# Kernel tuning notes

Measured on AMD Instinct MI355X. Metric: run time of the kernel, lower is better.

The kernel has to match this reference:

```python
import jax, jax.numpy as jnp
import numpy as np

MAX_SEQ, D, VOCAB, N_LAYERS = 2048, 256, 240, 6
DH = 64.0  # scale used inside RelativeGlobalAttention
BATCH = 4


def _pos_embedding():
    # sin(pow(pos*1e-5, i/D) - pi/2 * ((i+1)%2)), exactly as in __init__
    pos = np.arange(MAX_SEQ, dtype=np.float64)[:, None]
    i = np.arange(D, dtype=np.float64)[None, :]
    ang = np.power(pos * 1e-5, i / D) - np.pi * 0.5 * ((i + 1) % 2)
    return jnp.asarray(np.sin(ang), dtype=jnp.float32)  # [L, D]


def _skew(QE):
    # pad a zero column in front, reshape [B,L,L+1]->[B,L+1,L], drop first row
    B, L, _ = QE.shape
    cat = jnp.concatenate([jnp.zeros((B, L, 1), QE.dtype), QE], axis=2)
    return cat.reshape(B, L + 1, L)[:, 1:, :]


def _rel_attn(x, Wq, Wk, Wv):
    Q = x @ Wq  # [B,L,D]
    K = x @ Wk
    V = x @ Wv
    QE = jnp.einsum('bld,bmd->blm', Q, K - Q)      # Q @ (K-Q)^T
    Srel = _skew(QE)
    QKt = jnp.einsum('bld,bmd->blm', Q, K)
    scores = (QKt + Srel) / jnp.sqrt(jnp.asarray(DH, x.dtype))
    probs = jax.nn.softmax(scores, axis=-1)        # no causal mask in source
    return probs @ V


def setup_inputs() -> dict:
    key = jax.random.key(0)
    ks = jax.random.split(key, 16)
    s = 1.0 / np.sqrt(D)
    mk = lambda k, shape, sc: (jax.random.normal(k, shape, jnp.float32) * sc)
    inp = {
        'tokens': jax.random.randint(ks[0], (BATCH, MAX_SEQ), 0, VOCAB),
        'embed_table': mk(ks[1], (VOCAB, D), 0.05),
        'Wq1': mk(ks[2], (N_LAYERS, D, D), s),
        'Wk1': mk(ks[3], (N_LAYERS, D, D), s),
        'Wv1': mk(ks[4], (N_LAYERS, D, D), s),
        'Wq2': mk(ks[5], (N_LAYERS, D, D), s),
        'Wk2': mk(ks[6], (N_LAYERS, D, D), s),
        'Wv2': mk(ks[7], (N_LAYERS, D, D), s),
        'Wf1': mk(ks[8], (N_LAYERS, D, D), s),
        'bf1': jnp.zeros((N_LAYERS, D), jnp.float32),
        'Wf2': mk(ks[9], (N_LAYERS, D, D), s),
        'bf2': jnp.zeros((N_LAYERS, D), jnp.float32),
        'Wfc': mk(ks[10], (MAX_SEQ * D, VOCAB), 1.0 / np.sqrt(MAX_SEQ * D)),
        'bfc': jnp.zeros((VOCAB,), jnp.float32),
    }
    return inp


def reference(tokens, embed_table, Wq1, Wk1, Wv1, Wq2, Wk2, Wv2,
              Wf1, bf1, Wf2, bf2, Wfc, bfc):
    x = embed_table[tokens] + _pos_embedding()[None]  # [B,L,D]
    for i in range(N_LAYERS):
        x = _rel_attn(x, Wq1[i], Wk1[i], Wv1[i]) + x
        x = _rel_attn(x, Wq2[i], Wk2[i], Wv2[i]) + x
        h = jax.nn.leaky_relu(x @ Wf1[i] + bf1[i], negative_slope=0.2)
        x = h @ Wf2[i] + bf2[i]
        # NOTE: BatchNorm layers exist in source but are never called in _decoder
    flat = x.reshape(x.shape[0], -1)  # [B, L*D]
    return jax.nn.softmax(flat @ Wfc + bfc, axis=-1)  # [B, vocab]
```

## Files before the change

kernel.cpp:

```cpp
#include <hip/hip_runtime.h>
#include <hip/hip_fp16.h>

typedef unsigned short u16;
typedef unsigned int   u32;

#define BB 4
#define LL 2048
#define DD 256
#define VV 240
#define NLAYERS 6

static constexpr long BLD = (long)BB * LL * DD;
static constexpr long LD_ = (long)LL * DD;
static constexpr long LxL = (long)LL * LL;
static constexpr long BLL = (long)BB * LxL;

typedef _Float16 h8  __attribute__((ext_vector_type(8)));
typedef _Float16 h2v __attribute__((ext_vector_type(2)));
typedef float  f32x4 __attribute__((ext_vector_type(4)));

__device__ __forceinline__ u16 f2h(float f) {
    _Float16 h = (_Float16)f;
    return __builtin_bit_cast(u16, h);
}
__device__ __forceinline__ float h2f(u16 u) {
    return (float)__builtin_bit_cast(_Float16, u);
}

__device__ __forceinline__ void gl16(const void* g, void* l) {
    __builtin_amdgcn_global_load_lds((const __attribute__((address_space(1))) void*)g,
                                     (__attribute__((address_space(3))) void*)l, 16, 0, 0);
}

__global__ __launch_bounds__(256)
void embed_kernel(const int* __restrict__ tokens, const float* __restrict__ table,
                  float* __restrict__ x, u16* __restrict__ xh)
{
    long idx = (long)blockIdx.x * 256 + threadIdx.x;
    if (idx >= BLD) return;
    int i  = (int)(idx & (DD - 1));
    long bl = idx >> 8;
    int l  = (int)(bl & (LL - 1));
    int tok = tokens[bl];
    float base = (float)l * 1e-5f;
    float p = powf(base, (float)i * (1.0f / (float)DD));
    float ang = p - ((i & 1) ? 0.0f : 1.57079632679489662f);
    float v = table[(long)tok * DD + i] + sinf(ang);
    x[idx] = v;
    xh[idx] = f2h(v);
}

__global__ __launch_bounds__(256)
void wconv(const float* __restrict__ W, u16* __restrict__ Wt, long lstride)
{
    int blk = blockIdx.x;
    int m  = blk >> 6;
    int ti = (blk >> 3) & 7;
    int tj = blk & 7;
    const float* src = W + (long)m * 65536;
    u16* dst = Wt + (long)m * lstride;
    __shared__ float tile[32][33];
    int t = threadIdx.x;
    int c = t & 31, r8 = t >> 5;
    #pragma unroll
    for (int p = 0; p < 4; ++p) {
        int r = r8 + p * 8;
        tile[r][c] = src[(long)(ti * 32 + r) * 256 + tj * 32 + c];
    }
    __syncthreads();
    #pragma unroll
    for (int p = 0; p < 4; ++p) {
        int n = r8 + p * 8;
        dst[(long)(tj * 32 + n) * 256 + ti * 32 + c] = f2h(tile[c][n]);
    }
}

__global__ __launch_bounds__(256)
void sub_f16(u16* __restrict__ kk, const u16* __restrict__ q)
{
    long i = (long)blockIdx.x * 256 + threadIdx.x;
    uint4 kv = ((const uint4*)kk)[i];
    uint4 qv = ((const uint4*)q)[i];
    u32* kp = (u32*)&kv; const u32* qp = (const u32*)&qv;
    #pragma unroll
    for (int j = 0; j < 4; ++j) {
        h2v a = __builtin_bit_cast(h2v, kp[j]);
        h2v b = __builtin_bit_cast(h2v, qp[j]);
        h2v e = a - b;
        kp[j] = __builtin_bit_cast(u32, e);
    }
    ((uint4*)kk)[i] = kv;
}

template<int EPI, int BM, int BN>
__global__ __launch_bounds__(256)
void gemm_mfma(const u16* __restrict__ A, const u16* __restrict__ B,
               const float* __restrict__ bias, const float* __restrict__ Cres,
               float* __restrict__ Cf, u16* __restrict__ Ch,
               u16* __restrict__ Ch2, u16* __restrict__ Ch3,
               int M, int N, int K, int ldA,
               long sA, long sB, long sC)
{
    constexpr int FM = BM / 32, FN = BN / 32;
    __shared__ u16 As[BM * 32];
    __shared__ u16 Bs[BN * 32];
    const int bz = blockIdx.z;
    A += (long)bz * sA;
    B += (long)bz * sB;
    if constexpr (EPI & 4)  Cres += (long)bz * sC;
    if constexpr (EPI & 8)  Cf   += (long)bz * sC;
    if constexpr ((EPI & 16) && !(EPI & (32 | 64))) Ch += (long)bz * sC;
    const int bm = blockIdx.y * BM;
    const int bn = blockIdx.x * BN;
    const int t = threadIdx.x;
    const int lane = t & 63, wave = t >> 6;
    const int wm = (wave >> 1) * (BM / 2), wn = (wave & 1) * (BN / 2);

    f32x4 acc[FM][FN];
    #pragma unroll
    for (int i = 0; i < FM; ++i)
        #pragma unroll
        for (int j = 0; j < FN; ++j)
            acc[i][j] = (f32x4){0.f, 0.f, 0.f, 0.f};

    const u16* gA0 = A + (long)(bm + (t >> 2)) * ldA + (t & 3) * 8;
    const u16* gB0 = B + (long)(bn + (t >> 2)) * K + (t & 3) * 8;
    u16* lA0 = As + wave * 512;
    u16* lB0 = Bs + wave * 512;

    const int arow = wm + (lane & 15);
    const int brow = wn + (lane & 15);
    const int ko = (lane >> 4) * 8;

    for (int k0 = 0; k0 < K; k0 += 32) {
        __syncthreads();
        gl16(gA0, lA0);
        if constexpr (BM == 128) gl16(gA0 + 64L * ldA, As + 2048 + wave * 512);
        gl16(gB0, lB0);
        if constexpr (BN == 128) gl16(gB0 + 64L * K, Bs + 2048 + wave * 512);
        gA0 += 32; gB0 += 32;
        __syncthreads();
        h8 af[FM], bf[FN];
        #pragma unroll
        for (int i = 0; i < FM; ++i) af[i] = *(const h8*)&As[(arow + i * 16) * 32 + ko];
        #pragma unroll
        for (int j = 0; j < FN; ++j) bf[j] = *(const h8*)&Bs[(brow + j * 16) * 32 + ko];
        #pragma unroll
        for (int i = 0; i < FM; ++i)
            #pragma unroll
            for (int j = 0; j < FN; ++j)
                acc[i][j] = __builtin_amdgcn_mfma_f32_16x16x32_f16(af[i], bf[j], acc[i][j], 0, 0, 0);
    }

    const int colc = lane & 15;
    const int rowb = (lane >> 4) * 4;
    if constexpr (EPI & 64) {
        const int seg = bn >> 8;
        const int nb  = bn & 255;
        if (seg < 2) {
            u16* dst = seg ? Ch2 : Ch;
            #pragma unroll
            for (int i = 0; i < FM; ++i)
                #pragma unroll
                for (int j = 0; j < FN; ++j) {
                    int nn = nb + wn + j * 16 + colc;
                    #pragma unroll
                    for (int r = 0; r < 4; ++r) {
                        long row = bm + wm + i * 16 + rowb + r;
                        dst[row * DD + nn] = f2h(acc[i][j][r]);
                    }
                }
        } else {
            #pragma unroll
            for (int i = 0; i < FM; ++i) {
                int r0 = bm + wm + i * 16 + rowb;
                int b  = r0 >> 11;
                int m0 = r0 & (LL - 1);
                #pragma unroll
                for (int j = 0; j < FN; ++j) {
                    int nn = nb + wn + j * 16 + colc;
                    f32x4 v = acc[i][j];
                    ushort4 pk;
                    pk.x = f2h(v.x); pk.y = f2h(v.y); pk.z = f2h(v.z); pk.w = f2h(v.w);
                    *(ushort4*)&Ch3[((long)b * DD + nn) * LL + m0] = pk;
                }
            }
        }
    } else if constexpr (EPI & 32) {
        #pragma unroll
        for (int i = 0; i < FM; ++i) {
            int r0 = bm + wm + i * 16 + rowb;
            int b  = r0 >> 11;
            int m0 = r0 & (LL - 1);
            #pragma unroll
            for (int j = 0; j < FN; ++j) {
                int n = bn + wn + j * 16 + colc;
                f32x4 v = acc[i][j];
                ushort4 pk;
                pk.x = f2h(v.x); pk.y = f2h(v.y); pk.z = f2h(v.z); pk.w = f2h(v.w);
                *(ushort4*)&Ch[((long)b * DD + n) * LL + m0] = pk;
            }
        }
    } else {
        #pragma unroll
        for (int i = 0; i < FM; ++i) {
            #pragma unroll
            for (int j = 0; j < FN; ++j) {
                int n = bn + wn + j * 16 + colc;
                float bv = (EPI & 1) ? bias[n] : 0.f;
                #pragma unroll
                for (int r = 0; r < 4; ++r) {
                    long row = bm + wm + i * 16 + rowb + r;
                    float val = acc[i][j][r] + bv;
                    if (EPI & 2) val = (val >= 0.f) ? val : 0.2f * val;
                    long off = row * (long)N + n;
                    if (EPI & 4) val += Cres[off];
                    if (EPI & 8) Cf[off] = val;
                    if (EPI & 16) Ch[off] = f2h(val);
                }
            }
        }
    }
}

__global__ __launch_bounds__(256)
void skew_softmax(u16* __restrict__ S1, const u16* __restrict__ QE)
{
    const int bi = blockIdx.x;
    const int b = bi >> 11;
    const int i = bi & (LL - 1);
    u16* srow = S1 + (long)bi * LL;
    const u16* qe_i  = QE + ((long)b * LL + i) * LL;
    const u16* qe_i1 = qe_i + ((i + 1 < LL) ? LL : 0);
    const int t = threadIdx.x;

    uint4 sv = ((const uint4*)srow)[t];
    const u16* se = (const u16*)&sv;
    float vals[8];
    float mx = -1e30f;
    #pragma unroll
    for (int j = 0; j < 8; ++j) {
        int m = t * 8 + j;
        float srel;
        if (m <= i)            srel = h2f(qe_i[m - i + (LL - 1)]);
        else if (m == i + 1)   srel = 0.f;
        else                   srel = h2f(qe_i1[m - i - 2]);
        float s = (h2f(se[j]) + srel) * 0.125f;
        vals[j] = s;
        mx = fmaxf(mx, s);
    }
    #pragma unroll
    for (int off = 32; off >= 1; off >>= 1)
        mx = fmaxf(mx, __shfl_xor(mx, off, 64));
    __shared__ float redm[4], reds[4];
    const int wid = t >> 6;
    if ((t & 63) == 0) redm[wid] = mx;
    __syncthreads();
    mx = fmaxf(fmaxf(redm[0], redm[1]), fmaxf(redm[2], redm[3]));

    float sum = 0.f;
    #pragma unroll
    for (int j = 0; j < 8; ++j) { vals[j] = expf(vals[j] - mx); sum += vals[j]; }
    #pragma unroll
    for (int off = 32; off >= 1; off >>= 1)
        sum += __shfl_xor(sum, off, 64);
    if ((t & 63) == 0) reds[wid] = sum;
    __syncthreads();
    sum = reds[0] + reds[1] + reds[2] + reds[3];
    float inv = 1.0f / sum;
    uint4 ov;
    u16* oe = (u16*)&ov;
    #pragma unroll
    for (int j = 0; j < 8; ++j) oe[j] = f2h(vals[j] * inv);
    ((uint4*)srow)[t] = ov;
}

__global__ __launch_bounds__(960)
void fc_partial(const float* __restrict__ x, const float* __restrict__ W,
                float* __restrict__ part)
{
    const int v = threadIdx.x;
    const int b = threadIdx.y;
    const int chunk = blockIdx.x;
    const int KC = (int)(LD_ / 256);
    const long k0 = (long)chunk * KC;
    const float* xb = x + (long)b * LD_ + k0;
    const float* Wp = W + k0 * VV + v;
    float acc = 0.f;
    #pragma unroll 4
    for (int k2 = 0; k2 < KC; ++k2)
        acc = fmaf(xb[k2], Wp[(long)k2 * VV], acc);
    part[((long)chunk * BB + b) * VV + v] = acc;
}

__global__ __launch_bounds__(960)
void fc_finish(const float* __restrict__ part, const float* __restrict__ bias,
               float* __restrict__ out)
{
    const int v = threadIdx.x, b = threadIdx.y;
    float acc = bias[v];
    for (int c = 0; c < 256; ++c)
        acc += part[((long)c * BB + b) * VV + v];
    __shared__ float lds[BB][VV];
    __shared__ float mxs[BB], sms[BB];
    lds[b][v] = acc;
    __syncthreads();
    if (v == 0) {
        float m = -1e30f;
        for (int j = 0; j < VV; ++j) m = fmaxf(m, lds[b][j]);
        float s = 0.f;
        for (int j = 0; j < VV; ++j) s += expf(lds[b][j] - m);
        mxs[b] = m; sms[b] = s;
    }
    __syncthreads();
    out[b * VV + v] = expf(lds[b][v] - mxs[b]) / sms[b];
}

extern "C" void kernel_launch(void* const* d_in, const int* in_sizes, int n_in,
                              void* d_out, int out_size, void* d_ws, size_t ws_size,
                              hipStream_t stream)
{
    const int*   tokens = (const int*)d_in[0];
    const float* table  = (const float*)d_in[1];
    const float* Wq1 = (const float*)d_in[2];
    const float* Wk1 = (const float*)d_in[3];
    const float* Wv1 = (const float*)d_in[4];
    const float* Wq2 = (const float*)d_in[5];
    const float* Wk2 = (const float*)d_in[6];
    const float* Wv2 = (const float*)d_in[7];
    const float* Wf1 = (const float*)d_in[8];
    const float* bf1 = (const float*)d_in[9];
    const float* Wf2 = (const float*)d_in[10];
    const float* bf2 = (const float*)d_in[11];
    const float* Wfc = (const float*)d_in[12];
    const float* bfc = (const float*)d_in[13];

    char* p = (char*)d_ws;
    float* x  = (float*)p; p += BLD * 4;
    u16* xh = (u16*)p;     p += BLD * 2;
    u16* qb = (u16*)p;     p += BLD * 2;
    u16* kb = (u16*)p;     p += BLD * 2;
    u16* vt = (u16*)p;     p += BLD * 2;
    u16* S1 = (u16*)p;     p += BLL * 2;
    u16* QE = (u16*)p;     p += BLL * 2;
    u16* qkvw = (u16*)p;   p += 12L * 3 * 65536 * 2;
    u16* fw = (u16*)p;     p += 12L * 65536 * 2;
    float* part = (float*)p;
    u16* hb = qb;

    wconv<<<384, 256, 0, stream>>>(Wq1, qkvw + 0L * 65536,            3 * 65536);
    wconv<<<384, 256, 0, stream>>>(Wk1, qkvw + 1L * 65536,            3 * 65536);
    wconv<<<384, 256, 0, stream>>>(Wv1, qkvw + 2L * 65536,            3 * 65536);
    wconv<<<384, 256, 0, stream>>>(Wq2, qkvw + 18L * 65536,           3 * 65536);
    wconv<<<384, 256, 0, stream>>>(Wk2, qkvw + 18L * 65536 + 65536,   3 * 65536);
    wconv<<<384, 256, 0, stream>>>(Wv2, qkvw + 18L * 65536 + 2 * 65536, 3 * 65536);
    wconv<<<384, 256, 0, stream>>>(Wf1, fw, 65536);
    wconv<<<384, 256, 0, stream>>>(Wf2, fw + 6L * 65536, 65536);

    embed_kernel<<<(int)((BLD + 255) / 256), 256, 0, stream>>>(tokens, table, x, xh);

    const dim3 gqkv(6, 64, 1);
    const dim3 gscore(16, 16, BB);
    const dim3 gpv(4, 32, BB);
    const dim3 gffn(4, 128, 1);

    for (int layer = 0; layer < NLAYERS; ++layer) {
        for (int half = 0; half < 2; ++half) {
            const u16* wqkv = qkvw + ((long)(half * 6 + layer)) * 3 * 65536;
            gemm_mfma<64, 128, 128><<<gqkv, 256, 0, stream>>>(
                xh, wqkv, nullptr, nullptr, nullptr, qb, kb, vt,
                BB * LL, 768, DD, DD, 0, 0, 0);
            gemm_mfma<16, 128, 128><<<gscore, 256, 0, stream>>>(
                qb, kb, nullptr, nullptr, nullptr, S1, nullptr, nullptr,
                LL, LL, DD, DD, LD_, LD_, LxL);
            sub_f16<<<(int)(BLD / 8 / 256), 256, 0, stream>>>(kb, qb);
            gemm_mfma<16, 128, 128><<<gscore, 256, 0, stream>>>(
                qb, kb, nullptr, nullptr, nullptr, QE, nullptr, nullptr,
                LL, LL, DD, DD, LD_, LD_, LxL);
            skew_softmax<<<BB * LL, 256, 0, stream>>>(S1, QE);
            gemm_mfma<4 | 8 | 16, 64, 64><<<gpv, 256, 0, stream>>>(
                S1, vt, nullptr, x, x, xh, nullptr, nullptr,
                LL, DD, LL, LL, LxL, LD_, LD_);
        }
        gemm_mfma<1 | 2 | 16, 64, 64><<<gffn, 256, 0, stream>>>(
            xh, fw + (long)layer * 65536, bf1 + layer * DD, nullptr,
            nullptr, hb, nullptr, nullptr, BB * LL, DD, DD, DD, 0, 0, 0);
        gemm_mfma<1 | 8 | 16, 64, 64><<<gffn, 256, 0, stream>>>(
            hb, fw + (long)(6 + layer) * 65536, bf2 + layer * DD, nullptr,
            x, xh, nullptr, nullptr, BB * LL, DD, DD, DD, 0, 0, 0);
    }

    fc_partial<<<256, dim3(VV, BB, 1), 0, stream>>>(x, Wfc, part);
    fc_finish<<<1, dim3(VV, BB, 1), 0, stream>>>(part, bfc, (float*)d_out);
}
```

Measured before the change: 1.912 ms.

## Fold K-Q into weights, fuse both score GEMMs, double-buffer GEMM LDS

Computes K-Q directly as x@(Wk-Wq) by adding a difference weight to the fused projection GEMM, which removes the separate fp16 subtraction kernel. The two score GEMMs (Q@K^T and Q@(K-Q)^T) become one launch with twice the grid, each block picking its B operand and output by column range. The GEMM main loop now double-buffers its LDS tiles so the next K-slice load is issued before the current MFMAs, with one barrier per iteration instead of two. This trades a little extra projection work and rounding differences in E for fewer launches and some load/compute overlap.

```diff
diff --git a/kernel.cpp b/kernel.cpp
--- a/kernel.cpp
+++ b/kernel.cpp
@@ -16,7 +16,6 @@
 static constexpr long BLL = (long)BB * LxL;
 
 typedef _Float16 h8  __attribute__((ext_vector_type(8)));
-typedef _Float16 h2v __attribute__((ext_vector_type(2)));
 typedef float  f32x4 __attribute__((ext_vector_type(4)));
 
 __device__ __forceinline__ u16 f2h(float f) {
@@ -50,8 +49,10 @@
     xh[idx] = f2h(v);
 }
 
+template<bool DIFF>
 __global__ __launch_bounds__(256)
-void wconv(const float* __restrict__ W, u16* __restrict__ Wt, long lstride)
+void wconv(const float* __restrict__ W, const float* __restrict__ Wsub,
+           u16* __restrict__ Wt, long lstride)
 {
     int blk = blockIdx.x;
     int m  = blk >> 6;
@@ -65,7 +66,10 @@
     #pragma unroll
     for (int p = 0; p < 4; ++p) {
         int r = r8 + p * 8;
-        tile[r][c] = src[(long)(ti * 32 + r) * 256 + tj * 32 + c];
+        long off = (long)(ti * 32 + r) * 256 + tj * 32 + c;
+        float v = src[off];
+        if constexpr (DIFF) v -= Wsub[(long)m * 65536 + off];
+        tile[r][c] = v;
     }
     __syncthreads();
     #pragma unroll
@@ -75,43 +79,36 @@
     }
 }
 
-__global__ __launch_bounds__(256)
-void sub_f16(u16* __restrict__ kk, const u16* __restrict__ q)
-{
-    long i = (long)blockIdx.x * 256 + threadIdx.x;
-    uint4 kv = ((const uint4*)kk)[i];
-    uint4 qv = ((const uint4*)q)[i];
-    u32* kp = (u32*)&kv; const u32* qp = (const u32*)&qv;
-    #pragma unroll
-    for (int j = 0; j < 4; ++j) {
-        h2v a = __builtin_bit_cast(h2v, kp[j]);
-        h2v b = __builtin_bit_cast(h2v, qp[j]);
-        h2v e = a - b;
-        kp[j] = __builtin_bit_cast(u32, e);
-    }
-    ((uint4*)kk)[i] = kv;
-}
-
 template<int EPI, int BM, int BN>
 __global__ __launch_bounds__(256)
 void gemm_mfma(const u16* __restrict__ A, const u16* __restrict__ B,
+               const u16* __restrict__ B2,
                const float* __restrict__ bias, const float* __restrict__ Cres,
                float* __restrict__ Cf, u16* __restrict__ Ch,
-               u16* __restrict__ Ch2, u16* __restrict__ Ch3,
+               u16* __restrict__ Ch2, u16* __restrict__ Ch3, u16* __restrict__ Ch4,
                int M, int N, int K, int ldA,
                long sA, long sB, long sC)
 {
     constexpr int FM = BM / 32, FN = BN / 32;
-    __shared__ u16 As[BM * 32];
-    __shared__ u16 Bs[BN * 32];
+    __shared__ u16 As[2][BM * 32];
+    __shared__ u16 Bs[2][BN * 32];
     const int bz = blockIdx.z;
     A += (long)bz * sA;
-    B += (long)bz * sB;
+    const int bm = blockIdx.y * BM;
+    const int bn = blockIdx.x * BN;
+    int bnb = bn;
+    const u16* Bp;
+    if constexpr (EPI & 128) {
+        Bp = (bn >= LL) ? B2 : B;
+        if (bn >= LL) bnb = bn - LL;
+        Bp += (long)bz * sB;
+    } else {
+        Bp = B + (long)bz * sB;
+    }
     if constexpr (EPI & 4)  Cres += (long)bz * sC;
     if constexpr (EPI & 8)  Cf   += (long)bz * sC;
-    if constexpr ((EPI & 16) && !(EPI & (32 | 64))) Ch += (long)bz * sC;
-    const int bm = blockIdx.y * BM;
-    const int bn = blockIdx.x * BN;
+    if constexpr ((EPI & 16) && !(EPI & (64 | 128))) Ch += (long)bz * sC;
+
     const int t = threadIdx.x;
     const int lane = t & 63, wave = t >> 6;
     const int wm = (wave >> 1) * (BM / 2), wn = (wave & 1) * (BN / 2);
@@ -123,42 +120,51 @@
         for (int j = 0; j < FN; ++j)
             acc[i][j] = (f32x4){0.f, 0.f, 0.f, 0.f};
 
-    const u16* gA0 = A + (long)(bm + (t >> 2)) * ldA + (t & 3) * 8;
-    const u16* gB0 = B + (long)(bn + (t >> 2)) * K + (t & 3) * 8;
-    u16* lA0 = As + wave * 512;
-    u16* lB0 = Bs + wave * 512;
+    const u16* gA0 = A  + (long)(bm  + (t >> 2)) * ldA + (t & 3) * 8;
+    const u16* gB0 = Bp + (long)(bnb + (t >> 2)) * K   + (t & 3) * 8;
 
     const int arow = wm + (lane & 15);
     const int brow = wn + (lane & 15);
     const int ko = (lane >> 4) * 8;
 
+    #define STAGE(buf, koff) do {                                              \
+        gl16(gA0 + (koff), &As[buf][wave * 512]);                              \
+        if constexpr (BM == 128) gl16(gA0 + 64L * ldA + (koff),                \
+                                      &As[buf][2048 + wave * 512]);            \
+        gl16(gB0 + (koff), &Bs[buf][wave * 512]);                              \
+        if constexpr (BN == 128) gl16(gB0 + 64L * K + (koff),                  \
+                                      &Bs[buf][2048 + wave * 512]);            \
+    } while (0)
+
+    STAGE(0, 0);
+    int cur = 0;
     for (int k0 = 0; k0 < K; k0 += 32) {
         __syncthreads();
-        gl16(gA0, lA0);
-        if constexpr (BM == 128) gl16(gA0 + 64L * ldA, As + 2048 + wave * 512);
-        gl16(gB0, lB0);
-        if constexpr (BN == 128) gl16(gB0 + 64L * K, Bs + 2048 + wave * 512);
-        gA0 += 32; gB0 += 32;
-        __syncthreads();
+        if (k0 + 32 < K) {
+            if (cur) STAGE(0, k0 + 32);
+            else     STAGE(1, k0 + 32);
+        }
         h8 af[FM], bf[FN];
         #pragma unroll
-        for (int i = 0; i < FM; ++i) af[i] = *(const h8*)&As[(arow + i * 16) * 32 + ko];
-        #pragma unroll
-        for (int j = 0; j < FN; ++j) bf[j] = *(const h8*)&Bs[(brow + j * 16) * 32 + ko];
+        for (int i = 0; i < FM; ++i) af[i] = *(const h8*)&As[cur][(arow + i * 16) * 32 + ko];
+        #pragma unroll
+        for (int j = 0; j < FN; ++j) bf[j] = *(const h8*)&Bs[cur][(brow + j * 16) * 32 + ko];
         #pragma unroll
         for (int i = 0; i < FM; ++i)
             #pragma unroll
             for (int j = 0; j < FN; ++j)
                 acc[i][j] = __builtin_amdgcn_mfma_f32_16x16x32_f16(af[i], bf[j], acc[i][j], 0, 0, 0);
-    }
+        cur ^= 1;
+    }
+    #undef STAGE
 
     const int colc = lane & 15;
     const int rowb = (lane >> 4) * 4;
     if constexpr (EPI & 64) {
         const int seg = bn >> 8;
         const int nb  = bn & 255;
-        if (seg < 2) {
-            u16* dst = seg ? Ch2 : Ch;
+        if (seg < 3) {
+            u16* dst = (seg == 0) ? Ch : ((seg == 1) ? Ch2 : Ch3);
             #pragma unroll
             for (int i = 0; i < FM; ++i)
                 #pragma unroll
@@ -182,25 +188,24 @@
                     f32x4 v = acc[i][j];
                     ushort4 pk;
                     pk.x = f2h(v.x); pk.y = f2h(v.y); pk.z = f2h(v.z); pk.w = f2h(v.w);
-                    *(ushort4*)&Ch3[((long)b * DD + nn) * LL + m0] = pk;
+                    *(ushort4*)&Ch4[((long)b * DD + nn) * LL + m0] = pk;
                 }
             }
         }
-    } else if constexpr (EPI & 32) {
-        #pragma unroll
-        for (int i = 0; i < FM; ++i) {
-            int r0 = bm + wm + i * 16 + rowb;
-            int b  = r0 >> 11;
-            int m0 = r0 & (LL - 1);
+    } else if constexpr (EPI & 128) {
+        u16* dst = ((bn >= LL) ? Ch2 : Ch) + (long)bz * sC;
+        const int nb = bn & (LL - 1);
+        #pragma unroll
+        for (int i = 0; i < FM; ++i)
             #pragma unroll
             for (int j = 0; j < FN; ++j) {
-                int n = bn + wn + j * 16 + colc;
-                f32x4 v = acc[i][j];
-                ushort4 pk;
-                pk.x = f2h(v.x); pk.y = f2h(v.y); pk.z = f2h(v.z); pk.w = f2h(v.w);
-                *(ushort4*)&Ch[((long)b * DD + n) * LL + m0] = pk;
+                int n = nb + wn + j * 16 + colc;
+                #pragma unroll
+                for (int r = 0; r < 4; ++r) {
+                    long row = bm + wm + i * 16 + rowb + r;
+                    dst[row * LL + n] = f2h(acc[i][j][r]);
+                }
             }
-        }
     } else {
         #pragma unroll
         for (int i = 0; i < FM; ++i) {
@@ -340,54 +345,54 @@
     u16* xh = (u16*)p;     p += BLD * 2;
     u16* qb = (u16*)p;     p += BLD * 2;
     u16* kb = (u16*)p;     p += BLD * 2;
+    u16* eb = (u16*)p;     p += BLD * 2;
     u16* vt = (u16*)p;     p += BLD * 2;
     u16* S1 = (u16*)p;     p += BLL * 2;
     u16* QE = (u16*)p;     p += BLL * 2;
-    u16* qkvw = (u16*)p;   p += 12L * 3 * 65536 * 2;
+    u16* qkevw = (u16*)p;  p += 12L * 4 * 65536 * 2;
     u16* fw = (u16*)p;     p += 12L * 65536 * 2;
     float* part = (float*)p;
     u16* hb = qb;
 
-    wconv<<<384, 256, 0, stream>>>(Wq1, qkvw + 0L * 65536,            3 * 65536);
-    wconv<<<384, 256, 0, stream>>>(Wk1, qkvw + 1L * 65536,            3 * 65536);
-    wconv<<<384, 256, 0, stream>>>(Wv1, qkvw + 2L * 65536,            3 * 65536);
-    wconv<<<384, 256, 0, stream>>>(Wq2, qkvw + 18L * 65536,           3 * 65536);
-    wconv<<<384, 256, 0, stream>>>(Wk2, qkvw + 18L * 65536 + 65536,   3 * 65536);
-    wconv<<<384, 256, 0, stream>>>(Wv2, qkvw + 18L * 65536 + 2 * 65536, 3 * 65536);
-    wconv<<<384, 256, 0, stream>>>(Wf1, fw, 65536);
-    wconv<<<384, 256, 0, stream>>>(Wf2, fw + 6L * 65536, 65536);
+    const long LS = 4 * 65536;
+    wconv<false><<<384, 256, 0, stream>>>(Wq1, nullptr, qkevw + 0L * 65536, LS);
+    wconv<false><<<384, 256, 0, stream>>>(Wk1, nullptr, qkevw + 1L * 65536, LS);
+    wconv<true ><<<384, 256, 0, stream>>>(Wk1, Wq1,     qkevw + 2L * 65536, LS);
+    wconv<false><<<384, 256, 0, stream>>>(Wv1, nullptr, qkevw + 3L * 65536, LS);
+    wconv<false><<<384, 256, 0, stream>>>(Wq2, nullptr, qkevw + 24L * 65536, LS);
+    wconv<true ><<<384, 256, 0, stream>>>(Wk2, Wq2,     qkevw + 24L * 65536 + 2 * 65536, LS);
+    wconv<false><<<384, 256, 0, stream>>>(Wk2, nullptr, qkevw + 24L * 65536 + 1 * 65536, LS);
+    wconv<false><<<384, 256, 0, stream>>>(Wv2, nullptr, qkevw + 24L * 65536 + 3 * 65536, LS);
+    wconv<false><<<384, 256, 0, stream>>>(Wf1, nullptr, fw, 65536);
+    wconv<false><<<384, 256, 0, stream>>>(Wf2, nullptr, fw + 6L * 65536, 65536);
 
     embed_kernel<<<(int)((BLD + 255) / 256), 256, 0, stream>>>(tokens, table, x, xh);
 
-    const dim3 gqkv(6, 64, 1);
-    const dim3 gscore(16, 16, BB);
+    const dim3 gqkev(8, 64, 1);
+    const dim3 gscore(32, 16, BB);
     const dim3 gpv(4, 32, BB);
     const dim3 gffn(4, 128, 1);
 
     for (int layer = 0; layer < NLAYERS; ++layer) {
         for (int half = 0; half < 2; ++half) {
-            const u16* wqkv = qkvw + ((long)(half * 6 + layer)) * 3 * 65536;
-            gemm_mfma<64, 128, 128><<<gqkv, 256, 0, stream>>>(
-                xh, wqkv, nullptr, nullptr, nullptr, qb, kb, vt,
-                BB * LL, 768, DD, DD, 0, 0, 0);
-            gemm_mfma<16, 128, 128><<<gscore, 256, 0, stream>>>(
-                qb, kb, nullptr, nullptr, nullptr, S1, nullptr, nullptr,
-                LL, LL, DD, DD, LD_, LD_, LxL);
-            sub_f16<<<(int)(BLD / 8 / 256), 256, 0, stream>>>(kb, qb);
-            gemm_mfma<16, 128, 128><<<gscore, 256, 0, stream>>>(
-                qb, kb, nullptr, nullptr, nullptr, QE, nullptr, nullptr,
+            const u16* wqkev = qkevw + ((long)(half * 6 + layer)) * LS;
+            gemm_mfma<64, 128, 128><<<gqkev, 256, 0, stream>>>(
+                xh, wqkev, nullptr, nullptr, nullptr, nullptr, qb, kb, eb, vt,
+                BB * LL, 1024, DD, DD, 0, 0, 0);
+            gemm_mfma<128, 128, 128><<<gscore, 256, 0, stream>>>(
+                qb, kb, eb, nullptr, nullptr, nullptr, S1, QE, nullptr, nullptr,
                 LL, LL, DD, DD, LD_, LD_, LxL);
             skew_softmax<<<BB * LL, 256, 0, stream>>>(S1, QE);
             gemm_mfma<4 | 8 | 16, 64, 64><<<gpv, 256, 0, stream>>>(
-                S1, vt, nullptr, x, x, xh, nullptr, nullptr,
+                S1, vt, nullptr, nullptr, x, x, xh, nullptr, nullptr, nullptr,
                 LL, DD, LL, LL, LxL, LD_, LD_);
         }
         gemm_mfma<1 | 2 | 16, 64, 64><<<gffn, 256, 0, stream>>>(
-            xh, fw + (long)layer * 65536, bf1 + layer * DD, nullptr,
-            nullptr, hb, nullptr, nullptr, BB * LL, DD, DD, DD, 0, 0, 0);
+            xh, fw + (long)layer * 65536, nullptr, bf1 + layer * DD, nullptr,
+            nullptr, hb, nullptr, nullptr, nullptr, BB * LL, DD, DD, DD, 0, 0, 0);
         gemm_mfma<1 | 8 | 16, 64, 64><<<gffn, 256, 0, stream>>>(
-            hb, fw + (long)(6 + layer) * 65536, bf2 + layer * DD, nullptr,
-            x, xh, nullptr, nullptr, BB * LL, DD, DD, DD, 0, 0, 0);
+            hb, fw + (long)(6 + layer) * 65536, nullptr, bf2 + layer * DD, nullptr,
+            x, xh, nullptr, nullptr, nullptr, BB * LL, DD, DD, DD, 0, 0, 0);
     }
 
     fc_partial<<<256, dim3(VV, BB, 1), 0, stream>>>(x, Wfc, part);
```

Measured after the change: 1.783 ms. -6.7%, faster.
